# Kernel tuning notes

Hardware: AMD Instinct MI355X
Metric: run time of the kernel (lower is better)

## Reference

```python
import jax, jax.numpy as jnp
import numpy as np

SET_NUM, SET_SIZE, C, H, F, L_LAYERS, N_BLOCKS = 2048, 36, 192, 8, 384, 8, 4
N = SET_NUM * SET_SIZE


def _ln(x, g, b, eps=1e-5):
    m = x.mean(-1, keepdims=True)
    v = ((x - m) ** 2).mean(-1, keepdims=True)
    return (x - m) * jax.lax.rsqrt(v + eps) * g + b


def setup_inputs() -> dict:
    key = jax.random.key(0)
    ks = jax.random.split(key, 32)
    src = jax.random.normal(ks[0], (N, C), dtype=jnp.float32)
    pos_embed = jax.random.normal(ks[1], (2, N, C), dtype=jnp.float32)
    # each (shift, set) index tensor is a permutation of arange(N) -> every voxel appears exactly once
    perms = [jax.random.permutation(ks[2 + j], N).reshape(SET_NUM, SET_SIZE) for j in range(4)]
    set_voxel_inds = jnp.stack([jnp.stack(perms[0:2]), jnp.stack(perms[2:4])]).astype(jnp.int32)
    set_voxel_masks = jnp.zeros((2, 2, SET_NUM, SET_SIZE), dtype=bool)

    def p(k, shape, std=0.02):
        return (jax.random.normal(k, shape) * std).astype(jnp.float32)

    inp = dict(src=src, pos_embed=pos_embed, set_voxel_inds=set_voxel_inds,
               set_voxel_masks=set_voxel_masks,
               in_proj_w=p(ks[6], (L_LAYERS, 3 * C, C)), in_proj_b=p(ks[7], (L_LAYERS, 3 * C)),
               out_w=p(ks[8], (L_LAYERS, C, C)), out_b=p(ks[9], (L_LAYERS, C)),
               lin1_w=p(ks[10], (L_LAYERS, F, C)), lin1_b=p(ks[11], (L_LAYERS, F)),
               lin2_w=p(ks[12], (L_LAYERS, C, F)), lin2_b=p(ks[13], (L_LAYERS, C)),
               ln1_g=jnp.ones((L_LAYERS, C)), ln1_b=jnp.zeros((L_LAYERS, C)),
               ln2_g=jnp.ones((L_LAYERS, C)), ln2_b=jnp.zeros((L_LAYERS, C)),
               enc_g=jnp.ones((L_LAYERS, C)), enc_b=jnp.zeros((L_LAYERS, C)),
               blk_g=jnp.ones((N_BLOCKS, C)), blk_b=jnp.zeros((N_BLOCKS, C)))
    return inp


def reference(src, pos_embed, set_voxel_inds, set_voxel_masks,
              in_proj_w, in_proj_b, out_w, out_b, lin1_w, lin1_b, lin2_w, lin2_b,
              ln1_g, ln1_b, ln2_g, ln2_b, enc_g, enc_b, blk_g, blk_b):
    n_vox = src.shape[0]
    Dh = C // H
    scale = 1.0 / np.sqrt(Dh)

    def set_attn(x, pos, inds, mask, li):
        g = x[inds]                      # (S,K,C) gather voxels into sets
        qk_in = g + pos[inds]
        Wq, Wk, Wv = jnp.split(in_proj_w[li], 3, axis=0)
        bq, bk, bv = jnp.split(in_proj_b[li], 3)
        S, K = inds.shape
        q = (qk_in @ Wq.T + bq).reshape(S, K, H, Dh)
        k = (qk_in @ Wk.T + bk).reshape(S, K, H, Dh)
        v = (g @ Wv.T + bv).reshape(S, K, H, Dh)
        scores = jnp.einsum('skhd,slhd->shkl', q, k) * scale
        scores = jnp.where(mask[:, None, None, :], -1e9, scores)
        attn = jax.nn.softmax(scores, axis=-1)
        o = jnp.einsum('shkl,slhd->skhd', attn, v).reshape(S, K, C)
        o = o @ out_w[li].T + out_b[li]
        # torch.unique + flipped scatter == take the first occurrence of each voxel index
        flat = inds.reshape(-1)
        first = jnp.full((n_vox,), flat.size, dtype=flat.dtype).at[flat].min(
            jnp.arange(flat.size, dtype=flat.dtype))
        src2 = o.reshape(-1, C)[first]
        x = _ln(x + src2, ln1_g[li], ln1_b[li])
        ff = jax.nn.gelu(x @ lin1_w[li].T + lin1_b[li], approximate=False) @ lin2_w[li].T + lin2_b[li]
        x = _ln(x + ff, ln2_g[li], ln2_b[li])
        return x

    out = src
    for block_id in range(N_BLOCKS):
        residual = out
        shift = block_id % 2
        for i in range(2):
            li = block_id * 2 + i
            identity = out
            out = set_attn(out, pos_embed[i], set_voxel_inds[shift, i],
                           set_voxel_masks[shift, i], li)
            out = _ln(out + identity, enc_g[li], enc_b[li])
        out = _ln(out + residual, blk_g[block_id], blk_b[block_id])
    return out
```

## Files before the change

### kernel.cpp

```cpp
#include <hip/hip_runtime.h>
#include <hip/hip_bf16.h>
#include <hip/hip_fp16.h>

#define SETS 2048
#define SS   36
#define CDIM 192
#define HEADS 8
#define DH   24
#define FDIM 384
#define NVOX (SETS*SS)
#define NBLOCKS 4

typedef __hip_bfloat16 bf16;
typedef _Float16 f16;
typedef __attribute__((ext_vector_type(2))) _Float16 h2v;
typedef __attribute__((ext_vector_type(8))) short s8v;
typedef __attribute__((ext_vector_type(4))) float f4v;

__device__ __forceinline__ float to_f(float x) { return x; }
__device__ __forceinline__ float to_f(bf16 x)  { return __bfloat162float(x); }

__device__ __forceinline__ short f2bf(float x) {
  bf16 h = __float2bfloat16(x);
  return *reinterpret_cast<short*>(&h);
}
__device__ __forceinline__ float bfbits(unsigned short s) {
  unsigned u = ((unsigned)s) << 16;
  return __uint_as_float(u);
}
__device__ __forceinline__ void unpack2(unsigned w, float& a, float& b) {
  a = __uint_as_float(w << 16);
  b = __uint_as_float(w & 0xffff0000u);
}
__device__ __forceinline__ unsigned pack2(float a, float b) {
  return ((unsigned)(unsigned short)f2bf(a)) | (((unsigned)(unsigned short)f2bf(b)) << 16);
}

__device__ __forceinline__ float dot2(unsigned a, unsigned b, float acc) {
#if __has_builtin(__builtin_amdgcn_fdot2)
  return __builtin_amdgcn_fdot2(__builtin_bit_cast(h2v, a), __builtin_bit_cast(h2v, b), acc, false);
#else
  h2v ha = __builtin_bit_cast(h2v, a), hb = __builtin_bit_cast(h2v, b);
  return acc + (float)ha[0] * (float)hb[0] + (float)ha[1] * (float)hb[1];
#endif
}
__device__ __forceinline__ unsigned pkh(float a, float b) {
#if __has_builtin(__builtin_amdgcn_cvt_pkrtz)
  return __builtin_bit_cast(unsigned, __builtin_amdgcn_cvt_pkrtz(a, b));
#else
  h2v h; h[0] = (f16)a; h[1] = (f16)b;
  return __builtin_bit_cast(unsigned, h);
#endif
}
__device__ __forceinline__ unsigned permw(unsigned a, unsigned b, unsigned sel) {
#if __has_builtin(__builtin_amdgcn_perm)
  return __builtin_amdgcn_perm(b, a, sel);
#else
  if (sel == 0x05040100u) return (a & 0xffffu) | (b << 16);
  return (a >> 16) | (b & 0xffff0000u);
#endif
}

__device__ __forceinline__ float allreduce64(float v) {
  #pragma unroll
  for (int off = 32; off > 0; off >>= 1) v += __shfl_xor(v, off);
  return v;
}

__device__ __forceinline__ void ln3(float v[3], const float* g, const float* b, int t) {
  float s = allreduce64(v[0] + v[1] + v[2]);
  float m = s * (1.0f / 192.0f);
  float d0 = v[0] - m, d1 = v[1] - m, d2 = v[2] - m;
  float q = allreduce64(d0 * d0 + d1 * d1 + d2 * d2);
  float rs = rsqrtf(q * (1.0f / 192.0f) + 1e-5f);
  v[0] = d0 * rs * g[t]       + b[t];
  v[1] = d1 * rs * g[t + 64]  + b[t + 64];
  v[2] = d2 * rs * g[t + 128] + b[t + 128];
}

__global__ void copy_f4_k(const float4* __restrict__ in, float4* __restrict__ out) {
  int i = blockIdx.x * 256 + threadIdx.x;
  out[i] = in[i];
}

template<typename TO> __device__ __forceinline__ TO fcast(float v);
template<> __device__ __forceinline__ bf16 fcast<bf16>(float v) { return __float2bfloat16(v); }
template<> __device__ __forceinline__ f16  fcast<f16>(float v)  { return (f16)v; }

template<typename TA, typename TO, int BN, bool GATHER, bool ADD_POS, bool GELU_ACT>
__global__ __launch_bounds__(256) void mgemm_k(
    const TA* __restrict__ A, const float* __restrict__ W,
    const float* __restrict__ bias, TO* __restrict__ Cmat,
    const int* __restrict__ idx, const float* __restrict__ pos,
    int K, int ldc, int c_off)
{
  constexpr int BM = 128, LD = 40;
  constexpr int MI = (BN == 128) ? 4 : 2;
  constexpr bool A_F32 = (sizeof(TA) == 4);
  __shared__ short As[BM * LD];
  __shared__ short Bs[BN * LD];

  const int tid = threadIdx.x;
  const int n0 = blockIdx.x * BN;
  const int m0 = blockIdx.y * BM;
  const int wave = tid >> 6, lane = tid & 63;
  const int quad = lane >> 4, l16 = lane & 15;
  const int wm = (BN == 128) ? (wave >> 1) * 64 : wave * 32;
  const int wn = (BN == 128) ? (wave & 1) * 64 : 0;

  const int ar = tid >> 1;
  const int ah = (tid & 1) * 16;
  long arow = GATHER ? (long)idx[m0 + ar] : (long)(m0 + ar);
  const TA*    Ap = A + arow * (long)K;
  const float* Pp = ADD_POS ? (pos + arow * (long)K) : nullptr;

  const int br = (BN == 128) ? (tid >> 1) : (tid >> 2);
  const int bh = (BN == 128) ? (tid & 1) * 16 : (tid & 3) * 8;
  const float* Wp = W + (long)(n0 + br) * K;

  f4v acc[MI][4];
  #pragma unroll
  for (int i = 0; i < MI; i++)
    #pragma unroll
    for (int j = 0; j < 4; j++)
      #pragma unroll
      for (int r = 0; r < 4; r++) acc[i][j][r] = 0.f;

  for (int k0 = 0; k0 < K; k0 += 32) {
    {
      short* dst = &As[ar * LD + ah];
      if (A_F32 || ADD_POS) {
        float v[16];
        if (A_F32) {
          const float4* p = (const float4*)((const float*)Ap + k0 + ah);
          #pragma unroll
          for (int i = 0; i < 4; i++) {
            float4 t = p[i];
            v[4*i] = t.x; v[4*i+1] = t.y; v[4*i+2] = t.z; v[4*i+3] = t.w;
          }
        } else {
          const uint4* p = (const uint4*)((const bf16*)Ap + k0 + ah);
          #pragma unroll
          for (int i = 0; i < 2; i++) {
            uint4 u = p[i];
            unsigned ws_[4] = {u.x, u.y, u.z, u.w};
            #pragma unroll
            for (int q = 0; q < 4; q++) {
              v[8*i + 2*q]     = bfbits((unsigned short)(ws_[q] & 0xffff));
              v[8*i + 2*q + 1] = bfbits((unsigned short)(ws_[q] >> 16));
            }
          }
        }
        if (ADD_POS) {
          const float4* p = (const float4*)(Pp + k0 + ah);
          #pragma unroll
          for (int i = 0; i < 4; i++) {
            float4 t = p[i];
            v[4*i] += t.x; v[4*i+1] += t.y; v[4*i+2] += t.z; v[4*i+3] += t.w;
          }
        }
        s8v o0, o1;
        #pragma unroll
        for (int i = 0; i < 8; i++) { o0[i] = f2bf(v[i]); o1[i] = f2bf(v[8+i]); }
        *(s8v*)(dst)     = o0;
        *(s8v*)(dst + 8) = o1;
      } else {
        const s8v* p = (const s8v*)((const bf16*)Ap + k0 + ah);
        *(s8v*)(dst)     = p[0];
        *(s8v*)(dst + 8) = p[1];
      }
    }
    if (BN == 128) {
      const float4* p = (const float4*)(Wp + k0 + bh);
      float v[16];
      #pragma unroll
      for (int i = 0; i < 4; i++) {
        float4 t = p[i];
        v[4*i] = t.x; v[4*i+1] = t.y; v[4*i+2] = t.z; v[4*i+3] = t.w;
      }
      s8v o0, o1;
      #pragma unroll
      for (int i = 0; i < 8; i++) { o0[i] = f2bf(v[i]); o1[i] = f2bf(v[8+i]); }
      short* dst = &Bs[br * LD + bh];
      *(s8v*)(dst)     = o0;
      *(s8v*)(dst + 8) = o1;
    } else {
      const float4* p = (const float4*)(Wp + k0 + bh);
      float4 t0 = p[0], t1 = p[1];
      s8v o0;
      o0[0] = f2bf(t0.x); o0[1] = f2bf(t0.y); o0[2] = f2bf(t0.z); o0[3] = f2bf(t0.w);
      o0[4] = f2bf(t1.x); o0[5] = f2bf(t1.y); o0[6] = f2bf(t1.z); o0[7] = f2bf(t1.w);
      *(s8v*)(&Bs[br * LD + bh]) = o0;
    }
    __syncthreads();

    s8v af[MI], bfr[4];
    #pragma unroll
    for (int i = 0; i < MI; i++)
      af[i] = *(const s8v*)&As[(wm + i * 16 + l16) * LD + quad * 8];
    #pragma unroll
    for (int j = 0; j < 4; j++)
      bfr[j] = *(const s8v*)&Bs[(wn + j * 16 + l16) * LD + quad * 8];
    #pragma unroll
    for (int i = 0; i < MI; i++)
      #pragma unroll
      for (int j = 0; j < 4; j++)
        acc[i][j] = __builtin_amdgcn_mfma_f32_16x16x32_bf16(af[i], bfr[j], acc[i][j], 0, 0, 0);
    __syncthreads();
  }

  #pragma unroll
  for (int j = 0; j < 4; j++) {
    int gn = n0 + wn + j * 16 + l16;
    float bj = bias[gn];
    #pragma unroll
    for (int i = 0; i < MI; i++) {
      #pragma unroll
      for (int r = 0; r < 4; r++) {
        int gm = m0 + wm + i * 16 + quad * 4 + r;
        float vv = acc[i][j][r] + bj;
        if (GELU_ACT) vv = 0.5f * vv * (1.0f + erff(vv * 0.70710678118654752f));
        Cmat[(long)gm * ldc + c_off + gn] = fcast<TO>(vv);
      }
    }
  }
}

#define KLD 392
__global__ __launch_bounds__(288) void attn_set_k(const f16* __restrict__ qkv,
                                                  bf16* __restrict__ o)
{
  __shared__ short kv[SS * KLD];
  const int s = blockIdx.x;
  const int tid = threadIdx.x;

  const int h = tid / SS;
  const int r = tid - h * SS;

  const uint4* qp = (const uint4*)(qkv + ((size_t)s * SS + r) * 576 + h * DH);
  uint4 uq0 = qp[0], uq1 = qp[1], uq2 = qp[2];

  const uint4* gp = (const uint4*)(qkv + (size_t)s * (SS * 576));
  uint4* ls = (uint4*)kv;
  #pragma unroll
  for (int i = 0; i < 6; i++) {
    int u = tid + i * 288;
    int row = u / 48;
    int c = u - row * 48;
    ls[row * 49 + c] = gp[row * 72 + 24 + c];
  }
  __syncthreads();

  unsigned qw[12] = { uq0.x, uq0.y, uq0.z, uq0.w,
                      uq1.x, uq1.y, uq1.z, uq1.w,
                      uq2.x, uq2.y, uq2.z, uq2.w };

  const float scale = 0.20412414523193154f;
  float sc[SS];
  #pragma unroll
  for (int l = 0; l < SS; l++) {
    const uint4* kp = (const uint4*)&kv[l * KLD + h * DH];
    uint4 u0 = kp[0], u1 = kp[1], u2 = kp[2];
    float a0 = 0.f, a1 = 0.f, a2 = 0.f;
    a0 = dot2(qw[0], u0.x, a0); a0 = dot2(qw[1], u0.y, a0);
    a0 = dot2(qw[2], u0.z, a0); a0 = dot2(qw[3], u0.w, a0);
    a1 = dot2(qw[4], u1.x, a1); a1 = dot2(qw[5], u1.y, a1);
    a1 = dot2(qw[6], u1.z, a1); a1 = dot2(qw[7], u1.w, a1);
    a2 = dot2(qw[8], u2.x, a2); a2 = dot2(qw[9], u2.y, a2);
    a2 = dot2(qw[10], u2.z, a2); a2 = dot2(qw[11], u2.w, a2);
    sc[l] = (a0 + a1 + a2) * scale;
  }

  float mx = -1e30f;
  #pragma unroll
  for (int l = 0; l < SS; l++) mx = fmaxf(mx, sc[l]);
  float sum = 0.f;
  #pragma unroll
  for (int l = 0; l < SS; l++) { float e = __expf(sc[l] - mx); sc[l] = e; sum += e; }
  float inv = 1.0f / sum;

  float ov[DH];
  #pragma unroll
  for (int d = 0; d < DH; d++) ov[d] = 0.f;
  #pragma unroll
  for (int lp = 0; lp < SS / 2; lp++) {
    const uint4* va = (const uint4*)&kv[(2 * lp) * KLD + 192 + h * DH];
    const uint4* vb = (const uint4*)&kv[(2 * lp + 1) * KLD + 192 + h * DH];
    unsigned pp = pkh(sc[2 * lp], sc[2 * lp + 1]);
    #pragma unroll
    for (int i = 0; i < 3; i++) {
      uint4 ua = va[i], ub = vb[i];
      unsigned wa[4] = { ua.x, ua.y, ua.z, ua.w };
      unsigned wb[4] = { ub.x, ub.y, ub.z, ub.w };
      #pragma unroll
      for (int j = 0; j < 4; j++) {
        unsigned lo = permw(wa[j], wb[j], 0x05040100u);
        unsigned hi = permw(wa[j], wb[j], 0x07060302u);
        ov[8*i + 2*j]     = dot2(pp, lo, ov[8*i + 2*j]);
        ov[8*i + 2*j + 1] = dot2(pp, hi, ov[8*i + 2*j + 1]);
      }
    }
  }

  uint4* op = (uint4*)(o + ((size_t)s * SS + r) * CDIM + h * DH);
  #pragma unroll
  for (int i = 0; i < 3; i++) {
    uint4 u;
    u.x = pack2(ov[8*i+0] * inv, ov[8*i+1] * inv);
    u.y = pack2(ov[8*i+2] * inv, ov[8*i+3] * inv);
    u.z = pack2(ov[8*i+4] * inv, ov[8*i+5] * inv);
    u.w = pack2(ov[8*i+6] * inv, ov[8*i+7] * inv);
    op[i] = u;
  }
}

__global__ __launch_bounds__(256) void scatter_ln1_k(
    const float* __restrict__ xin, const bf16* __restrict__ o2,
    const int* __restrict__ inds, const float* __restrict__ g,
    const float* __restrict__ b, float* __restrict__ x1)
{
  int p = blockIdx.x * 4 + (threadIdx.x >> 6);
  int t = threadIdx.x & 63;
  int vox = inds[p];
  long vb = (long)vox * 192, pb = (long)p * 192;
  float v[3];
  #pragma unroll
  for (int j = 0; j < 3; j++) { int c = t + 64 * j; v[j] = xin[vb + c] + to_f(o2[pb + c]); }
  ln3(v, g, b, t);
  #pragma unroll
  for (int j = 0; j < 3; j++) { int c = t + 64 * j; x1[vb + c] = v[j]; }
}

template<bool HAS_BLK, bool WRITE_OUT>
__global__ __launch_bounds__(256) void ln_chain_k(
    const float* __restrict__ x1, const bf16* __restrict__ ff,
    const float* __restrict__ identity, const float* __restrict__ resid,
    const float* __restrict__ g2, const float* __restrict__ b2,
    const float* __restrict__ ge, const float* __restrict__ be,
    const float* __restrict__ gb, const float* __restrict__ bb,
    float* __restrict__ outf, float* __restrict__ outd)
{
  int row = blockIdx.x * 4 + (threadIdx.x >> 6);
  int t = threadIdx.x & 63;
  long base = (long)row * 192;
  float v[3];
  #pragma unroll
  for (int j = 0; j < 3; j++) { int c = t + 64 * j; v[j] = x1[base + c] + to_f(ff[base + c]); }
  ln3(v, g2, b2, t);
  #pragma unroll
  for (int j = 0; j < 3; j++) { int c = t + 64 * j; v[j] += identity[base + c]; }
  ln3(v, ge, be, t);
  if (HAS_BLK) {
    #pragma unroll
    for (int j = 0; j < 3; j++) { int c = t + 64 * j; v[j] += resid[base + c]; }
    ln3(v, gb, bb, t);
  }
  #pragma unroll
  for (int j = 0; j < 3; j++) {
    int c = t + 64 * j;
    outf[base + c] = v[j];
    if (WRITE_OUT) outd[base + c] = v[j];
  }
}

extern "C" void kernel_launch(void* const* d_in, const int* in_sizes, int n_in,
                              void* d_out, int out_size, void* d_ws, size_t ws_size,
                              hipStream_t stream)
{
  const float* src       = (const float*)d_in[0];
  const float* pos_embed = (const float*)d_in[1];
  const int*   svi       = (const int*)d_in[2];
  const float* ipw  = (const float*)d_in[4];
  const float* ipb  = (const float*)d_in[5];
  const float* outw = (const float*)d_in[6];
  const float* outb = (const float*)d_in[7];
  const float* l1w  = (const float*)d_in[8];
  const float* l1b  = (const float*)d_in[9];
  const float* l2w  = (const float*)d_in[10];
  const float* l2b  = (const float*)d_in[11];
  const float* ln1g = (const float*)d_in[12];
  const float* ln1b = (const float*)d_in[13];
  const float* ln2g = (const float*)d_in[14];
  const float* ln2b = (const float*)d_in[15];
  const float* encg = (const float*)d_in[16];
  const float* encb = (const float*)d_in[17];
  const float* blkg = (const float*)d_in[18];
  const float* blkb = (const float*)d_in[19];

  char* w = (char*)d_ws;
  const size_t ACT  = (size_t)NVOX * CDIM * sizeof(float);
  const size_t QKVB = (size_t)NVOX * 576 * sizeof(f16);
  const size_t OB   = (size_t)NVOX * CDIM * sizeof(bf16);
  float* act[3] = { (float*)w, (float*)(w + ACT), (float*)(w + 2 * ACT) };
  f16*  qkv   = (f16*)(w + 3 * ACT);
  bf16* obuf  = (bf16*)(w + 3 * ACT + QKVB);
  bf16* o2buf = (bf16*)(w + 3 * ACT + QKVB + OB);
  bf16* hbuf  = (bf16*)qkv;
  bf16* ffbuf = obuf;

  copy_f4_k<<<NVOX * CDIM / 4 / 256, 256, 0, stream>>>((const float4*)src, (float4*)act[0]);

  int r = 0, ia = 1, ib = 2;
  for (int blkid = 0; blkid < NBLOCKS; blkid++) {
    int shift = blkid & 1;
    float* xres = act[r];
    float* cur  = act[r];
    float* outs[2] = { act[ia], act[ib] };
    for (int i = 0; i < 2; i++) {
      int li = blkid * 2 + i;
      const int* inds = svi + (size_t)(shift * 2 + i) * SETS * SS;
      const float* pos = pos_embed + (size_t)i * NVOX * CDIM;
      const float* Wip = ipw + (size_t)li * 576 * 192;
      const float* Bip = ipb + (size_t)li * 576;

      mgemm_k<float, f16, 128, true, true, false><<<dim3(3, NVOX / 128), 256, 0, stream>>>(
          cur, Wip, Bip, qkv, inds, pos, 192, 576, 0);
      mgemm_k<float, f16, 64, true, false, false><<<dim3(3, NVOX / 128), 256, 0, stream>>>(
          cur, Wip + 384 * 192, Bip + 384, qkv, inds, nullptr, 192, 576, 384);

      attn_set_k<<<SETS, 288, 0, stream>>>(qkv, obuf);

      mgemm_k<bf16, bf16, 64, false, false, false><<<dim3(3, NVOX / 128), 256, 0, stream>>>(
          obuf, outw + (size_t)li * 192 * 192, outb + (size_t)li * 192, o2buf,
          nullptr, nullptr, 192, 192, 0);

      float* x1 = outs[i];
      scatter_ln1_k<<<NVOX / 4, 256, 0, stream>>>(cur, o2buf, inds,
          ln1g + (size_t)li * 192, ln1b + (size_t)li * 192, x1);

      mgemm_k<float, bf16, 128, false, false, true><<<dim3(3, NVOX / 128), 256, 0, stream>>>(
          x1, l1w + (size_t)li * 384 * 192, l1b + (size_t)li * 384, hbuf,
          nullptr, nullptr, 192, 384, 0);
      mgemm_k<bf16, bf16, 64, false, false, false><<<dim3(3, NVOX / 128), 256, 0, stream>>>(
          hbuf, l2w + (size_t)li * 192 * 384, l2b + (size_t)li * 192, ffbuf,
          nullptr, nullptr, 384, 192, 0);

      bool isFinal = (blkid == NBLOCKS - 1 && i == 1);
      if (i == 1) {
        if (isFinal)
          ln_chain_k<true, true><<<NVOX / 4, 256, 0, stream>>>(x1, ffbuf, cur, xres,
              ln2g + (size_t)li * 192, ln2b + (size_t)li * 192,
              encg + (size_t)li * 192, encb + (size_t)li * 192,
              blkg + (size_t)blkid * 192, blkb + (size_t)blkid * 192,
              x1, (float*)d_out);
        else
          ln_chain_k<true, false><<<NVOX / 4, 256, 0, stream>>>(x1, ffbuf, cur, xres,
              ln2g + (size_t)li * 192, ln2b + (size_t)li * 192,
              encg + (size_t)li * 192, encb + (size_t)li * 192,
              blkg + (size_t)blkid * 192, blkb + (size_t)blkid * 192,
              x1, nullptr);
      } else {
        ln_chain_k<false, false><<<NVOX / 4, 256, 0, stream>>>(x1, ffbuf, cur, xres,
            ln2g + (size_t)li * 192, ln2b + (size_t)li * 192,
            encg + (size_t)li * 192, encb + (size_t)li * 192,
            nullptr, nullptr, x1, nullptr);
      }
      cur = x1;
    }
    int newr = ib, na = r, nb = ia;
    r = newr; ia = na; ib = nb;
  }
}
```

Measured before the change: 2.887 ms.

## Use full-width GEMM tiles and fuse Q/K and V projections into one kernel

The GEMM kernel now takes tile shape and wave layout as template parameters, so each block computes the full output width (576, 384 or 192 columns) over 64 rows. A is gathered and converted once per row and no longer re-read by three column blocks. The QK and V projections merge into one launch that stages both x+pos and x in shared memory and picks the operand per column tile. The cost is larger per-block shared memory and accumulator register footprint (512 threads, many accumulators), which may reduce occupancy, and the K loop still has no double buffering.

```diff
diff --git a/kernel.cpp b/kernel.cpp
--- a/kernel.cpp
+++ b/kernel.cpp
@@ -14,6 +14,7 @@
 typedef __hip_bfloat16 bf16;
 typedef _Float16 f16;
 typedef __attribute__((ext_vector_type(2))) _Float16 h2v;
+typedef __attribute__((ext_vector_type(4))) short s4v;
 typedef __attribute__((ext_vector_type(8))) short s8v;
 typedef __attribute__((ext_vector_type(4))) float f4v;
 
@@ -23,10 +24,6 @@
 __device__ __forceinline__ short f2bf(float x) {
   bf16 h = __float2bfloat16(x);
   return *reinterpret_cast<short*>(&h);
-}
-__device__ __forceinline__ float bfbits(unsigned short s) {
-  unsigned u = ((unsigned)s) << 16;
-  return __uint_as_float(u);
 }
 __device__ __forceinline__ void unpack2(unsigned w, float& a, float& b) {
   a = __uint_as_float(w << 16);
@@ -87,131 +84,112 @@
 template<> __device__ __forceinline__ bf16 fcast<bf16>(float v) { return __float2bfloat16(v); }
 template<> __device__ __forceinline__ f16  fcast<f16>(float v)  { return (f16)v; }
 
-template<typename TA, typename TO, int BN, bool GATHER, bool ADD_POS, bool GELU_ACT>
-__global__ __launch_bounds__(256) void mgemm_k(
+template<typename TA, typename TO, int BM, int BN, int WM, int WN,
+         bool GATHER, int POS_NCOL, bool GELU_ACT>
+__global__ __launch_bounds__(WM*WN*64, 4) void mgemm_k(
     const TA* __restrict__ A, const float* __restrict__ W,
     const float* __restrict__ bias, TO* __restrict__ Cmat,
     const int* __restrict__ idx, const float* __restrict__ pos,
-    int K, int ldc, int c_off)
+    int K, int ldc)
 {
-  constexpr int BM = 128, LD = 40;
-  constexpr int MI = (BN == 128) ? 4 : 2;
+  constexpr int NTHR = WM * WN * 64;
+  constexpr int LD = 40;
   constexpr bool A_F32 = (sizeof(TA) == 4);
+  constexpr bool DUAL  = (POS_NCOL > 0);
+  constexpr int MI  = BM / (16 * WM);
+  constexpr int NJ  = BN / (16 * WN);
+  constexpr int BCH = BN * 8 / NTHR;
+  static_assert(A_F32 ? (BM * 8 == NTHR) : (BM * 4 == NTHR), "A staging = 1 chunk");
+  static_assert(BN * 8 % NTHR == 0, "B staging chunks");
+
   __shared__ short As[BM * LD];
+  __shared__ short Asv[DUAL ? BM * LD : 8];
   __shared__ short Bs[BN * LD];
 
   const int tid = threadIdx.x;
-  const int n0 = blockIdx.x * BN;
   const int m0 = blockIdx.y * BM;
   const int wave = tid >> 6, lane = tid & 63;
   const int quad = lane >> 4, l16 = lane & 15;
-  const int wm = (BN == 128) ? (wave >> 1) * 64 : wave * 32;
-  const int wn = (BN == 128) ? (wave & 1) * 64 : 0;
-
-  const int ar = tid >> 1;
-  const int ah = (tid & 1) * 16;
+  const int wm = (wave / WN) * (BM / WM);
+  const int wn = (wave % WN) * (BN / WN);
+
+  const int ar  = A_F32 ? (tid >> 3) : (tid >> 2);
+  const int ac4 = A_F32 ? (tid & 7)  : (tid & 3);
   long arow = GATHER ? (long)idx[m0 + ar] : (long)(m0 + ar);
-  const TA*    Ap = A + arow * (long)K;
-  const float* Pp = ADD_POS ? (pos + arow * (long)K) : nullptr;
-
-  const int br = (BN == 128) ? (tid >> 1) : (tid >> 2);
-  const int bh = (BN == 128) ? (tid & 1) * 16 : (tid & 3) * 8;
-  const float* Wp = W + (long)(n0 + br) * K;
-
-  f4v acc[MI][4];
+  const TA*    Ap = A + arow * (long)K + (A_F32 ? ac4 * 4 : ac4 * 8);
+  const float* Pp = DUAL ? (pos + arow * (long)K + ac4 * 4) : nullptr;
+  const int aoff = ar * LD + (A_F32 ? ac4 * 4 : ac4 * 8);
+
+  const float* WpA[BCH];
+  int boff[BCH];
+  #pragma unroll
+  for (int c = 0; c < BCH; c++) {
+    int u = tid + c * NTHR;
+    int row = u >> 3, f4 = u & 7;
+    WpA[c] = W + (long)row * K + f4 * 4;
+    boff[c] = row * LD + f4 * 4;
+  }
+
+  f4v acc[MI][NJ];
   #pragma unroll
   for (int i = 0; i < MI; i++)
     #pragma unroll
-    for (int j = 0; j < 4; j++)
+    for (int j = 0; j < NJ; j++)
       #pragma unroll
       for (int r = 0; r < 4; r++) acc[i][j][r] = 0.f;
 
   for (int k0 = 0; k0 < K; k0 += 32) {
-    {
-      short* dst = &As[ar * LD + ah];
-      if (A_F32 || ADD_POS) {
-        float v[16];
-        if (A_F32) {
-          const float4* p = (const float4*)((const float*)Ap + k0 + ah);
-          #pragma unroll
-          for (int i = 0; i < 4; i++) {
-            float4 t = p[i];
-            v[4*i] = t.x; v[4*i+1] = t.y; v[4*i+2] = t.z; v[4*i+3] = t.w;
-          }
-        } else {
-          const uint4* p = (const uint4*)((const bf16*)Ap + k0 + ah);
-          #pragma unroll
-          for (int i = 0; i < 2; i++) {
-            uint4 u = p[i];
-            unsigned ws_[4] = {u.x, u.y, u.z, u.w};
-            #pragma unroll
-            for (int q = 0; q < 4; q++) {
-              v[8*i + 2*q]     = bfbits((unsigned short)(ws_[q] & 0xffff));
-              v[8*i + 2*q + 1] = bfbits((unsigned short)(ws_[q] >> 16));
-            }
-          }
-        }
-        if (ADD_POS) {
-          const float4* p = (const float4*)(Pp + k0 + ah);
-          #pragma unroll
-          for (int i = 0; i < 4; i++) {
-            float4 t = p[i];
-            v[4*i] += t.x; v[4*i+1] += t.y; v[4*i+2] += t.z; v[4*i+3] += t.w;
-          }
-        }
-        s8v o0, o1;
-        #pragma unroll
-        for (int i = 0; i < 8; i++) { o0[i] = f2bf(v[i]); o1[i] = f2bf(v[8+i]); }
-        *(s8v*)(dst)     = o0;
-        *(s8v*)(dst + 8) = o1;
+    if (A_F32) {
+      float4 tx = *(const float4*)((const float*)Ap + k0);
+      if (DUAL) {
+        float4 tp = *(const float4*)(Pp + k0);
+        s4v oq, ovv;
+        oq[0] = f2bf(tx.x + tp.x); oq[1] = f2bf(tx.y + tp.y);
+        oq[2] = f2bf(tx.z + tp.z); oq[3] = f2bf(tx.w + tp.w);
+        ovv[0] = f2bf(tx.x); ovv[1] = f2bf(tx.y);
+        ovv[2] = f2bf(tx.z); ovv[3] = f2bf(tx.w);
+        *(s4v*)&As[aoff]  = oq;
+        *(s4v*)&Asv[aoff] = ovv;
       } else {
-        const s8v* p = (const s8v*)((const bf16*)Ap + k0 + ah);
-        *(s8v*)(dst)     = p[0];
-        *(s8v*)(dst + 8) = p[1];
+        s4v o;
+        o[0] = f2bf(tx.x); o[1] = f2bf(tx.y); o[2] = f2bf(tx.z); o[3] = f2bf(tx.w);
+        *(s4v*)&As[aoff] = o;
       }
-    }
-    if (BN == 128) {
-      const float4* p = (const float4*)(Wp + k0 + bh);
-      float v[16];
+    } else {
+      *(uint4*)&As[aoff] = *(const uint4*)((const bf16*)Ap + k0);
+    }
+    #pragma unroll
+    for (int c = 0; c < BCH; c++) {
+      float4 t = *(const float4*)(WpA[c] + k0);
+      s4v o;
+      o[0] = f2bf(t.x); o[1] = f2bf(t.y); o[2] = f2bf(t.z); o[3] = f2bf(t.w);
+      *(s4v*)&Bs[boff[c]] = o;
+    }
+    __syncthreads();
+
+    s8v aq[MI], av[DUAL ? MI : 1];
+    #pragma unroll
+    for (int i = 0; i < MI; i++)
+      aq[i] = *(const s8v*)&As[(wm + i * 16 + l16) * LD + quad * 8];
+    if (DUAL)
       #pragma unroll
-      for (int i = 0; i < 4; i++) {
-        float4 t = p[i];
-        v[4*i] = t.x; v[4*i+1] = t.y; v[4*i+2] = t.z; v[4*i+3] = t.w;
-      }
-      s8v o0, o1;
+      for (int i = 0; i < MI; i++)
+        av[i] = *(const s8v*)&Asv[(wm + i * 16 + l16) * LD + quad * 8];
+    #pragma unroll
+    for (int j = 0; j < NJ; j++) {
+      s8v bfr = *(const s8v*)&Bs[(wn + j * 16 + l16) * LD + quad * 8];
+      const bool useq = !DUAL || (wn + j * 16) < POS_NCOL;
       #pragma unroll
-      for (int i = 0; i < 8; i++) { o0[i] = f2bf(v[i]); o1[i] = f2bf(v[8+i]); }
-      short* dst = &Bs[br * LD + bh];
-      *(s8v*)(dst)     = o0;
-      *(s8v*)(dst + 8) = o1;
-    } else {
-      const float4* p = (const float4*)(Wp + k0 + bh);
-      float4 t0 = p[0], t1 = p[1];
-      s8v o0;
-      o0[0] = f2bf(t0.x); o0[1] = f2bf(t0.y); o0[2] = f2bf(t0.z); o0[3] = f2bf(t0.w);
-      o0[4] = f2bf(t1.x); o0[5] = f2bf(t1.y); o0[6] = f2bf(t1.z); o0[7] = f2bf(t1.w);
-      *(s8v*)(&Bs[br * LD + bh]) = o0;
+      for (int i = 0; i < MI; i++)
+        acc[i][j] = __builtin_amdgcn_mfma_f32_16x16x32_bf16(useq ? aq[i] : av[i],
+                                                            bfr, acc[i][j], 0, 0, 0);
     }
     __syncthreads();
-
-    s8v af[MI], bfr[4];
-    #pragma unroll
-    for (int i = 0; i < MI; i++)
-      af[i] = *(const s8v*)&As[(wm + i * 16 + l16) * LD + quad * 8];
-    #pragma unroll
-    for (int j = 0; j < 4; j++)
-      bfr[j] = *(const s8v*)&Bs[(wn + j * 16 + l16) * LD + quad * 8];
-    #pragma unroll
-    for (int i = 0; i < MI; i++)
-      #pragma unroll
-      for (int j = 0; j < 4; j++)
-        acc[i][j] = __builtin_amdgcn_mfma_f32_16x16x32_bf16(af[i], bfr[j], acc[i][j], 0, 0, 0);
-    __syncthreads();
-  }
-
-  #pragma unroll
-  for (int j = 0; j < 4; j++) {
-    int gn = n0 + wn + j * 16 + l16;
+  }
+
+  #pragma unroll
+  for (int j = 0; j < NJ; j++) {
+    int gn = wn + j * 16 + l16;
     float bj = bias[gn];
     #pragma unroll
     for (int i = 0; i < MI; i++) {
@@ -220,7 +198,7 @@
         int gm = m0 + wm + i * 16 + quad * 4 + r;
         float vv = acc[i][j][r] + bj;
         if (GELU_ACT) vv = 0.5f * vv * (1.0f + erff(vv * 0.70710678118654752f));
-        Cmat[(long)gm * ldc + c_off + gn] = fcast<TO>(vv);
+        Cmat[(long)gm * ldc + gn] = fcast<TO>(vv);
       }
     }
   }
@@ -413,27 +391,29 @@
       const float* Wip = ipw + (size_t)li * 576 * 192;
       const float* Bip = ipb + (size_t)li * 576;
 
-      mgemm_k<float, f16, 128, true, true, false><<<dim3(3, NVOX / 128), 256, 0, stream>>>(
-          cur, Wip, Bip, qkv, inds, pos, 192, 576, 0);
-      mgemm_k<float, f16, 64, true, false, false><<<dim3(3, NVOX / 128), 256, 0, stream>>>(
-          cur, Wip + 384 * 192, Bip + 384, qkv, inds, nullptr, 192, 576, 384);
+      mgemm_k<float, f16, 64, 576, 2, 4, true, 384, false>
+          <<<dim3(1, NVOX / 64), 512, 0, stream>>>(
+          cur, Wip, Bip, qkv, inds, pos, 192, 576);
 
       attn_set_k<<<SETS, 288, 0, stream>>>(qkv, obuf);
 
-      mgemm_k<bf16, bf16, 64, false, false, false><<<dim3(3, NVOX / 128), 256, 0, stream>>>(
+      mgemm_k<bf16, bf16, 64, 192, 2, 2, false, 0, false>
+          <<<dim3(1, NVOX / 64), 256, 0, stream>>>(
           obuf, outw + (size_t)li * 192 * 192, outb + (size_t)li * 192, o2buf,
-          nullptr, nullptr, 192, 192, 0);
+          nullptr, nullptr, 192, 192);
 
       float* x1 = outs[i];
       scatter_ln1_k<<<NVOX / 4, 256, 0, stream>>>(cur, o2buf, inds,
           ln1g + (size_t)li * 192, ln1b + (size_t)li * 192, x1);
 
-      mgemm_k<float, bf16, 128, false, false, true><<<dim3(3, NVOX / 128), 256, 0, stream>>>(
+      mgemm_k<float, bf16, 64, 384, 2, 4, false, 0, true>
+          <<<dim3(1, NVOX / 64), 512, 0, stream>>>(
           x1, l1w + (size_t)li * 384 * 192, l1b + (size_t)li * 384, hbuf,
-          nullptr, nullptr, 192, 384, 0);
-      mgemm_k<bf16, bf16, 64, false, false, false><<<dim3(3, NVOX / 128), 256, 0, stream>>>(
+          nullptr, nullptr, 192, 384);
+      mgemm_k<bf16, bf16, 64, 192, 2, 2, false, 0, false>
+          <<<dim3(1, NVOX / 64), 256, 0, stream>>>(
           hbuf, l2w + (size_t)li * 192 * 384, l2b + (size_t)li * 192, ffbuf,
-          nullptr, nullptr, 384, 192, 0);
+          nullptr, nullptr, 384, 192);
 
       bool isFinal = (blkid == NBLOCKS - 1 && i == 1);
       if (i == 1) {
```

New measurement: 3.330 ms. 1.15x slower.
